# Kernel tuning notes

Hardware: AMD Instinct MI355X
Metric: run time of the kernel (lower is better)

Reference implementation:

```python
import jax, jax.numpy as jnp
import numpy as np

D_MODEL = 1024
NUM_HEADS = 16
HEAD_DIM = D_MODEL // NUM_HEADS


def setup_inputs() -> dict:
    key = jax.random.key(0)
    kx, kq, kk, kv, ko = jax.random.split(key, 5)
    B, S = 2, 2048
    scale = 1.0 / np.sqrt(D_MODEL)
    return {
        "x": jax.random.normal(kx, (B, S, D_MODEL), dtype=jnp.float32),
        "W_q": jax.random.normal(kq, (D_MODEL, D_MODEL), dtype=jnp.float32) * scale,
        "W_k": jax.random.normal(kk, (D_MODEL, D_MODEL), dtype=jnp.float32) * scale,
        "W_v": jax.random.normal(kv, (D_MODEL, D_MODEL), dtype=jnp.float32) * scale,
        "W_o": jax.random.normal(ko, (D_MODEL, D_MODEL), dtype=jnp.float32) * scale,
        "causal": 1,
    }


def _attn(x, W_q, W_k, W_v, W_o, causal):
    B, S, D = x.shape
    H, Hd = NUM_HEADS, HEAD_DIM
    # projections: nn.Linear applies x @ W.T
    q = (x @ W_q.T).reshape(B, S, H, Hd)
    k = (x @ W_k.T).reshape(B, S, H, Hd)
    v = (x @ W_v.T).reshape(B, S, H, Hd)
    # scores: [B, H, S, S]
    scores = jnp.einsum("bqhd,bkhd->bhqk", q, k) / np.sqrt(Hd)
    if causal:
        mask = jnp.triu(jnp.ones((S, S), dtype=bool), k=1)
        scores = jnp.where(mask, -jnp.inf, scores)
    attn = jax.nn.softmax(scores, axis=-1)
    out = jnp.einsum("bhqk,bkhd->bqhd", attn, v).reshape(B, S, D)
    return out @ W_o.T


def reference(x, W_q, W_k, W_v, W_o, causal):
    return _attn(x, W_q, W_k, W_v, W_o, causal)
```

## Files before the change

### kernel.cpp

```cpp
#include <hip/hip_runtime.h>

typedef __attribute__((ext_vector_type(8))) short bf16x8;
typedef __attribute__((ext_vector_type(4))) float f32x4;
typedef __attribute__((ext_vector_type(4))) unsigned short u16x4;

#define MFMA16(a, b, c) __builtin_amdgcn_mfma_f32_16x16x32_bf16((a), (b), (c), 0, 0, 0)

static constexpr int D_MODEL = 1024;
static constexpr int SEQ = 2048;
static constexpr int NH = 16;
static constexpr int HD = 64;
static constexpr int LDA = 40;
static constexpr int MST = 136;
static constexpr float NEG_BIG = -1.0e30f;

__device__ __forceinline__ unsigned short f2bf(float f) {
  union { float f; unsigned int u; } v; v.f = f;
  unsigned int r = v.u + 0x7fffu + ((v.u >> 16) & 1u);
  return (unsigned short)(r >> 16);
}

__device__ __forceinline__ unsigned int cvtpk_bf16(float a, float b) {
  unsigned int r;
  asm("v_cvt_pk_bf16_f32 %0, %1, %2" : "=v"(r) : "v"(a), "v"(b));
  return r;
}

__device__ __forceinline__ int detect_bf16(const unsigned short* xs, int lane) {
  unsigned short s = xs[2 * lane];
  int e = (s >> 7) & 0xFF;
  bool hit = (e >= 117 && e <= 129);
  unsigned long long m = __ballot(hit);
  return (__popcll(m) >= 32) ? 1 : 0;
}

__device__ __forceinline__ bf16x8 ld8(const void* p, size_t eidx, int bf) {
  if (bf) return *(const bf16x8*)((const unsigned short*)p + eidx);
  const float* f = (const float*)p + eidx;
  f32x4 lo = *(const f32x4*)f;
  f32x4 hi = *(const f32x4*)(f + 4);
  bf16x8 r;
  r[0] = (short)f2bf(lo[0]); r[1] = (short)f2bf(lo[1]);
  r[2] = (short)f2bf(lo[2]); r[3] = (short)f2bf(lo[3]);
  r[4] = (short)f2bf(hi[0]); r[5] = (short)f2bf(hi[1]);
  r[6] = (short)f2bf(hi[2]); r[7] = (short)f2bf(hi[3]);
  return r;
}

__device__ __forceinline__ void async16(const unsigned short* g, unsigned short* l) {
  __builtin_amdgcn_global_load_lds(
      (const __attribute__((address_space(1))) void*)g,
      (__attribute__((address_space(3))) void*)l, 16, 0, 0);
}

__global__ __launch_bounds__(64) void detect_kernel(
    const unsigned short* __restrict__ xs, int* __restrict__ flag) {
  int lane = threadIdx.x;
  unsigned short s = xs[2 * lane];
  int e = (s >> 7) & 0xFF;
  bool hit = (e >= 117 && e <= 129);
  unsigned long long m = __ballot(hit);
  if (lane == 0) { flag[0] = (__popcll(m) >= 32) ? 1 : 0; flag[1] = 1; }
}

__global__ __launch_bounds__(256) void convert_kernel(
    const void* __restrict__ X,
    const void* __restrict__ W0, const void* __restrict__ W1,
    const void* __restrict__ W2, const void* __restrict__ W3,
    unsigned short* __restrict__ Xb, unsigned short* __restrict__ Wb)
{
  const int bf = detect_bf16((const unsigned short*)X, threadIdx.x & 63);
  const int ty = blockIdx.y;
  const void* src; unsigned short* dst; size_t n;
  if (ty == 0) { src = X; dst = Xb; n = (size_t)2 * SEQ * D_MODEL; }
  else {
    src = (ty == 1) ? W0 : (ty == 2) ? W1 : (ty == 3) ? W2 : W3;
    dst = Wb + (size_t)(ty - 1) * D_MODEL * D_MODEL;
    n = (size_t)D_MODEL * D_MODEL;
  }
  size_t i = ((size_t)blockIdx.x * 256 + threadIdx.x) * 8;
  if (i >= n) return;
  *(bf16x8*)(dst + i) = ld8(src, i, bf);
}

__device__ __forceinline__ void gemm_fast_core(
    const unsigned short* __restrict__ A, const unsigned short* __restrict__ B,
    int tm, int tn, unsigned short* smem, f32x4 acc[4][4])
{
  const int t = threadIdx.x;
  const int lane = t & 63;
  const int w = t >> 6;
  const int wm = (w >> 1) * 64, wn = (w & 1) * 64;
  const int quad = lane >> 4, l16 = lane & 15;
  const int srow = lane >> 2;
  const int scol = ((lane & 3) ^ ((lane >> 3) & 3)) * 8;
  const int xa = (l16 >> 1) & 3;

#pragma unroll
  for (int mi = 0; mi < 4; ++mi)
#pragma unroll
    for (int ni = 0; ni < 4; ++ni)
      acc[mi][ni] = (f32x4){0.f, 0.f, 0.f, 0.f};

  auto stage = [&](int f, int buf) {
    const int k0 = f * 32;
    unsigned short* dst = smem + buf * 8192;
#pragma unroll
    for (int i = 0; i < 2; ++i) {
      const int row = w * 32 + i * 16;
      async16(A + (size_t)(tm + row + srow) * D_MODEL + k0 + scol,
              dst + row * 32);
      async16(B + (size_t)(tn + row + srow) * D_MODEL + k0 + scol,
              dst + 4096 + row * 32);
    }
  };

  stage(0, 0);
  stage(1, 1);

  int cur = 0, nb = 2;
  for (int f = 0; f < 32; ++f) {
    if (f + 1 < 32) asm volatile("s_waitcnt vmcnt(4)" ::: "memory");
    else            asm volatile("s_waitcnt vmcnt(0)" ::: "memory");
    __builtin_amdgcn_s_barrier();
    __builtin_amdgcn_sched_barrier(0);
    if (f + 2 < 32) stage(f + 2, nb);
    const unsigned short* As = smem + cur * 8192;
    const unsigned short* Bs = As + 4096;
    bf16x8 af[4], bfv[4];
#pragma unroll
    for (int mi = 0; mi < 4; ++mi)
      af[mi] = *(const bf16x8*)(As + (wm + mi * 16 + l16) * 32 + (quad ^ xa) * 8);
#pragma unroll
    for (int ni = 0; ni < 4; ++ni)
      bfv[ni] = *(const bf16x8*)(Bs + (wn + ni * 16 + l16) * 32 + (quad ^ xa) * 8);
    __builtin_amdgcn_s_setprio(1);
#pragma unroll
    for (int mi = 0; mi < 4; ++mi)
#pragma unroll
      for (int ni = 0; ni < 4; ++ni)
        acc[mi][ni] = MFMA16(af[mi], bfv[ni], acc[mi][ni]);
    __builtin_amdgcn_s_setprio(0);
    cur = (cur == 2) ? 0 : cur + 1;
    nb = (nb == 2) ? 0 : nb + 1;
  }
}

__global__ __launch_bounds__(256) void qkv_fast_kernel(
    const unsigned short* __restrict__ X,
    const unsigned short* __restrict__ Wb,
    unsigned short* __restrict__ qd,
    unsigned short* __restrict__ kws,
    unsigned short* __restrict__ vws)
{
  __shared__ __align__(16) unsigned short smem[3 * 8192];
  const int bid = blockIdx.x;
  const int xcd = bid & 7, s0 = bid >> 3;
  const int z = s0 >> 5;
  const int tn = ((s0 >> 2) & 7) * 128;
  const int tm = (xcd * 4 + (s0 & 3)) * 128;
  const unsigned short* W = Wb + (size_t)z * D_MODEL * D_MODEL;
  f32x4 acc[4][4];
  gemm_fast_core(X, W, tm, tn, smem, acc);

  const int t = threadIdx.x;
  const int lane = t & 63, w = t >> 6;
  const int wm = (w >> 1) * 64, wn = (w & 1) * 64;
  const int quad = lane >> 4, l16 = lane & 15;

  if (z == 2) {
    const int b = tm >> 11;
    const int sb = tm & 2047;
#pragma unroll
    for (int ph = 0; ph < 2; ++ph) {
      __syncthreads();
      if ((w & 1) == ph) {
#pragma unroll
        for (int mi = 0; mi < 4; ++mi)
#pragma unroll
          for (int ni = 0; ni < 4; ++ni)
#pragma unroll
            for (int r = 0; r < 4; ++r) {
              int m_local = wm + mi * 16 + quad * 4 + r;
              int n_sub = ni * 16 + l16;
              smem[n_sub * MST + m_local] = f2bf(acc[mi][ni][r]);
            }
      }
      __syncthreads();
      const int row = t >> 2, c0 = (t & 3) * 32;
      const int n_g = tn + ph * 64 + row;
      const int h = n_g >> 6, d = n_g & 63;
      unsigned short* dst = vws + (((size_t)b * NH + h) * HD + d) * SEQ + sb + c0;
#pragma unroll
      for (int cc = 0; cc < 4; ++cc)
        *(bf16x8*)(dst + cc * 8) = *(const bf16x8*)(smem + row * MST + c0 + cc * 8);
    }
    return;
  }
#pragma unroll
  for (int mi = 0; mi < 4; ++mi)
#pragma unroll
    for (int ni = 0; ni < 4; ++ni)
#pragma unroll
      for (int r = 0; r < 4; ++r) {
        int m = tm + wm + mi * 16 + quad * 4 + r;
        int n = tn + wn + ni * 16 + l16;
        unsigned short bv = f2bf(acc[mi][ni][r]);
        if (z == 0) {
          qd[(size_t)m * D_MODEL + n] = bv;
        } else {
          int b = m >> 11, sg = m & 2047;
          int h = n >> 6, d = n & 63;
          kws[(((size_t)b * NH + h) * SEQ + sg) * HD + d] = bv;
        }
      }
}

__global__ __launch_bounds__(256) void oproj_fast_kernel(
    const unsigned short* __restrict__ AW,
    const unsigned short* __restrict__ Wo,
    const unsigned short* __restrict__ Xorig,
    void* __restrict__ out)
{
  __shared__ __align__(16) unsigned short smem[3 * 8192];
  const int bf = detect_bf16(Xorig, threadIdx.x & 63);
  const int bid = blockIdx.x;
  const int xcd = bid & 7, s0 = bid >> 3;
  const int tmg = xcd >> 2, tng = xcd & 3;
  const int tm = (tmg * 16 + (s0 >> 1)) * 128;
  const int tn = (tng * 2 + (s0 & 1)) * 128;
  f32x4 acc[4][4];
  gemm_fast_core(AW, Wo, tm, tn, smem, acc);

  const int t = threadIdx.x;
  const int lane = t & 63, w = t >> 6;
  const int wm = (w >> 1) * 64, wn = (w & 1) * 64;
  const int quad = lane >> 4, l16 = lane & 15;
  if (bf) {
    unsigned short* o = (unsigned short*)out;
#pragma unroll
    for (int mi = 0; mi < 4; ++mi)
#pragma unroll
      for (int ni = 0; ni < 4; ++ni)
#pragma unroll
        for (int r = 0; r < 4; ++r) {
          int m = tm + wm + mi * 16 + quad * 4 + r;
          int n = tn + wn + ni * 16 + l16;
          o[(size_t)m * D_MODEL + n] = f2bf(acc[mi][ni][r]);
        }
  } else {
    float* o = (float*)out;
#pragma unroll
    for (int mi = 0; mi < 4; ++mi)
#pragma unroll
      for (int ni = 0; ni < 4; ++ni)
#pragma unroll
        for (int r = 0; r < 4; ++r) {
          int m = tm + wm + mi * 16 + quad * 4 + r;
          int n = tn + wn + ni * 16 + l16;
          o[(size_t)m * D_MODEL + n] = acc[mi][ni][r];
        }
  }
}

__device__ __forceinline__ void gemm_tile_128x128(
    const void* __restrict__ A, const void* __restrict__ B, int bf,
    int tm, int tn, unsigned short* As, unsigned short* Bs, f32x4 acc[4][4])
{
  const int t = threadIdx.x;
  const int lane = t & 63;
  const int w = t >> 6;
  const int wm = (w >> 1) * 64, wn = (w & 1) * 64;
  const int quad = lane >> 4, l16 = lane & 15;
  const int r0 = t >> 2, kc = (t & 3) * 8;
  const int r1 = r0 + 64;

#pragma unroll
  for (int mi = 0; mi < 4; ++mi)
#pragma unroll
    for (int ni = 0; ni < 4; ++ni)
      acc[mi][ni] = (f32x4){0.f, 0.f, 0.f, 0.f};

  for (int k0 = 0; k0 < D_MODEL; k0 += 32) {
    bf16x8 a0 = ld8(A, (size_t)(tm + r0) * D_MODEL + k0 + kc, bf);
    bf16x8 a1 = ld8(A, (size_t)(tm + r1) * D_MODEL + k0 + kc, bf);
    bf16x8 b0 = ld8(B, (size_t)(tn + r0) * D_MODEL + k0 + kc, bf);
    bf16x8 b1 = ld8(B, (size_t)(tn + r1) * D_MODEL + k0 + kc, bf);
    __syncthreads();
    *(bf16x8*)(As + r0 * LDA + kc) = a0;
    *(bf16x8*)(As + r1 * LDA + kc) = a1;
    *(bf16x8*)(Bs + r0 * LDA + kc) = b0;
    *(bf16x8*)(Bs + r1 * LDA + kc) = b1;
    __syncthreads();
    bf16x8 af[4], bfv[4];
#pragma unroll
    for (int mi = 0; mi < 4; ++mi)
      af[mi] = *(const bf16x8*)(As + (wm + mi * 16 + l16) * LDA + quad * 8);
#pragma unroll
    for (int ni = 0; ni < 4; ++ni)
      bfv[ni] = *(const bf16x8*)(Bs + (wn + ni * 16 + l16) * LDA + quad * 8);
#pragma unroll
    for (int mi = 0; mi < 4; ++mi)
#pragma unroll
      for (int ni = 0; ni < 4; ++ni)
        acc[mi][ni] = MFMA16(af[mi], bfv[ni], acc[mi][ni]);
  }
}

__global__ __launch_bounds__(256) void qkv_kernel(
    const void* __restrict__ X,
    const void* __restrict__ Wq,
    const void* __restrict__ Wk,
    const void* __restrict__ Wv,
    const int* __restrict__ flag,
    unsigned short* __restrict__ qd,
    unsigned short* __restrict__ kws,
    unsigned short* __restrict__ vws)
{
  __shared__ __align__(16) unsigned short As[128 * LDA];
  __shared__ __align__(16) unsigned short Bs[128 * LDA];
  const int bf = *flag;
  const int z = blockIdx.z;
  const void* W = (z == 0) ? Wq : ((z == 1) ? Wk : Wv);
  const int tm = blockIdx.y * 128, tn = blockIdx.x * 128;
  f32x4 acc[4][4];
  gemm_tile_128x128(X, W, bf, tm, tn, As, Bs, acc);

  const int t = threadIdx.x;
  const int lane = t & 63, w = t >> 6;
  const int wm = (w >> 1) * 64, wn = (w & 1) * 64;
  const int quad = lane >> 4, l16 = lane & 15;
#pragma unroll
  for (int mi = 0; mi < 4; ++mi)
#pragma unroll
    for (int ni = 0; ni < 4; ++ni)
#pragma unroll
      for (int r = 0; r < 4; ++r) {
        int m = tm + wm + mi * 16 + quad * 4 + r;
        int n = tn + wn + ni * 16 + l16;
        unsigned short bv = f2bf(acc[mi][ni][r]);
        if (z == 0) {
          qd[(size_t)m * D_MODEL + n] = bv;
        } else {
          int b = m >> 11, s = m & 2047;
          int h = n >> 6, d = n & 63;
          if (z == 1) kws[(((size_t)b * NH + h) * SEQ + s) * HD + d] = bv;
          else        vws[(((size_t)b * NH + h) * HD + d) * SEQ + s] = bv;
        }
      }
}

__global__ __launch_bounds__(256) void oproj_kernel(
    const unsigned short* __restrict__ AW,
    const void* __restrict__ Wo,
    const int* __restrict__ flag,
    float* __restrict__ tmp)
{
  __shared__ __align__(16) unsigned short As[128 * LDA];
  __shared__ __align__(16) unsigned short Bs[128 * LDA];
  const int bf = *flag;
  const int t = threadIdx.x;
  const int lane = t & 63;
  const int w = t >> 6;
  const int wm = (w >> 1) * 64, wn = (w & 1) * 64;
  const int quad = lane >> 4, l16 = lane & 15;
  const int r0 = t >> 2, kc = (t & 3) * 8;
  const int r1 = r0 + 64;
  const int tm = blockIdx.y * 128, tn = blockIdx.x * 128;
  f32x4 acc[4][4];
#pragma unroll
  for (int mi = 0; mi < 4; ++mi)
#pragma unroll
    for (int ni = 0; ni < 4; ++ni)
      acc[mi][ni] = (f32x4){0.f, 0.f, 0.f, 0.f};

  for (int k0 = 0; k0 < D_MODEL; k0 += 32) {
    bf16x8 a0 = *(const bf16x8*)(AW + (size_t)(tm + r0) * D_MODEL + k0 + kc);
    bf16x8 a1 = *(const bf16x8*)(AW + (size_t)(tm + r1) * D_MODEL + k0 + kc);
    bf16x8 b0 = ld8(Wo, (size_t)(tn + r0) * D_MODEL + k0 + kc, bf);
    bf16x8 b1 = ld8(Wo, (size_t)(tn + r1) * D_MODEL + k0 + kc, bf);
    __syncthreads();
    *(bf16x8*)(As + r0 * LDA + kc) = a0;
    *(bf16x8*)(As + r1 * LDA + kc) = a1;
    *(bf16x8*)(Bs + r0 * LDA + kc) = b0;
    *(bf16x8*)(Bs + r1 * LDA + kc) = b1;
    __syncthreads();
    bf16x8 af[4], bfv[4];
#pragma unroll
    for (int mi = 0; mi < 4; ++mi)
      af[mi] = *(const bf16x8*)(As + (wm + mi * 16 + l16) * LDA + quad * 8);
#pragma unroll
    for (int ni = 0; ni < 4; ++ni)
      bfv[ni] = *(const bf16x8*)(Bs + (wn + ni * 16 + l16) * LDA + quad * 8);
#pragma unroll
    for (int mi = 0; mi < 4; ++mi)
#pragma unroll
      for (int ni = 0; ni < 4; ++ni)
        acc[mi][ni] = MFMA16(af[mi], bfv[ni], acc[mi][ni]);
  }
#pragma unroll
  for (int mi = 0; mi < 4; ++mi)
#pragma unroll
    for (int ni = 0; ni < 4; ++ni)
#pragma unroll
      for (int r = 0; r < 4; ++r) {
        int m = tm + wm + mi * 16 + quad * 4 + r;
        int n = tn + wn + ni * 16 + l16;
        tmp[(size_t)m * D_MODEL + n] = acc[mi][ni][r];
      }
}

__device__ __forceinline__ void qk_part(
    const bf16x8 (&kfr)[4][2], const bf16x8 (&aq)[2], f32x4 (&sc)[4])
{
  __builtin_amdgcn_s_setprio(1);
#pragma unroll
  for (int cb = 0; cb < 4; ++cb) {
    sc[cb] = (f32x4){0.f, 0.f, 0.f, 0.f};
    sc[cb] = MFMA16(kfr[cb][0], aq[0], sc[cb]);
    sc[cb] = MFMA16(kfr[cb][1], aq[1], sc[cb]);
  }
  __builtin_amdgcn_s_setprio(0);
}

__device__ __forceinline__ void smpv_part(
    f32x4 (&sc)[4], const bf16x8 (&vfr)[4][2], f32x4 (&oacc)[4], float& lsum,
    int diag, int ktbase, int qq, int quad, float Cs)
{
  if (diag) {
#pragma unroll
    for (int cb = 0; cb < 4; ++cb)
#pragma unroll
      for (int rr = 0; rr < 4; ++rr)
        if (ktbase + (cb & 1) * 32 + quad * 8 + (cb >> 1) * 4 + rr > qq)
          sc[cb][rr] = NEG_BIG;
  }
#pragma unroll
  for (int cb = 0; cb < 4; ++cb)
#pragma unroll
    for (int rr = 0; rr < 4; ++rr)
      sc[cb][rr] = __builtin_amdgcn_exp2f(sc[cb][rr] * Cs);
  f32x4 t0, t1;
#pragma unroll
  for (int rr = 0; rr < 4; ++rr) { t0[rr] = sc[0][rr] + sc[1][rr]; }
#pragma unroll
  for (int rr = 0; rr < 4; ++rr) { t1[rr] = sc[2][rr] + sc[3][rr]; }
#pragma unroll
  for (int rr = 0; rr < 4; ++rr) { t0[rr] += t1[rr]; }
  lsum += (t0[0] + t0[1]) + (t0[2] + t0[3]);
  bf16x8 bp[2];
#pragma unroll
  for (int hf = 0; hf < 2; ++hf) {
    union { unsigned int w4[4]; bf16x8 v; } u;
    u.w4[0] = cvtpk_bf16(sc[hf][0], sc[hf][1]);
    u.w4[1] = cvtpk_bf16(sc[hf][2], sc[hf][3]);
    u.w4[2] = cvtpk_bf16(sc[2 + hf][0], sc[2 + hf][1]);
    u.w4[3] = cvtpk_bf16(sc[2 + hf][2], sc[2 + hf][3]);
    bp[hf] = u.v;
  }
  __builtin_amdgcn_s_setprio(1);
#pragma unroll
  for (int db = 0; db < 4; ++db) {
    oacc[db] = MFMA16(vfr[db][0], bp[0], oacc[db]);
    oacc[db] = MFMA16(vfr[db][1], bp[1], oacc[db]);
  }
  __builtin_amdgcn_s_setprio(0);
}

__global__ __launch_bounds__(256, 2) void attn_kernel(
    unsigned short* __restrict__ Qd,
    const unsigned short* __restrict__ Kb,
    const unsigned short* __restrict__ Vt,
    const int* __restrict__ causal_p)
{
  __shared__ __align__(16) unsigned short Ks[3][64 * 64];
  __shared__ __align__(16) unsigned short Vs[3][64 * 64];
  const int bid = blockIdx.x;
  const int xcd = bid & 7, slot = bid >> 3;
  const int bhl = slot >> 4;
  const int praw = slot & 15;
  const int p = (bhl & 2) ? (15 - praw) : praw;
  const int bh = xcd * 4 + bhl;
  const int b = bh >> 4, h = bh & 15;
  const int t = threadIdx.x, lane = t & 63, w = t >> 6;
  const int quad = lane >> 4, l16 = lane & 15;
  const int causal = *causal_p;
  const int tA = causal ? (31 - p) : (2 * p);
  const int tB = causal ? p : (2 * p + 1);
  const int ITEMS = causal ? (32 - p) : 32;
  unsigned short* qh = Qd + (size_t)b * SEQ * D_MODEL + h * HD;
  const unsigned short* kh = Kb + ((size_t)b * NH + h) * SEQ * HD;
  const unsigned short* vh = Vt + ((size_t)b * NH + h) * HD * SEQ;
  const float Cs = 0.125f * 1.4426950408889634f;
  const int srow = lane >> 3;
  const int gcol = ((lane & 7) ^ srow) * 8;
  const int xa = l16 & 7;

  int kvp[2];
#pragma unroll
  for (int j2 = 0; j2 < 2; ++j2) {
    const int rp = w * 16 + j2 * 8 + srow;
    kvp[j2] = ((rp >> 4) & 1) * 32 + ((rp >> 2) & 3) * 8 + ((rp >> 5) & 1) * 4 + (rp & 3);
  }

  const int qA = tA * 64 + w * 16, qB = tB * 64 + w * 16;
  bf16x8 aqA[2], aqB[2];
#pragma unroll
  for (int ch = 0; ch < 2; ++ch) {
    aqA[ch] = *(const bf16x8*)(qh + (size_t)(qA + l16) * D_MODEL +
                               ch * 32 + quad * 8);
    aqB[ch] = *(const bf16x8*)(qh + (size_t)(qB + l16) * D_MODEL +
                               ch * 32 + quad * 8);
  }

  f32x4 oaccA[4], oaccB[4];
#pragma unroll
  for (int db = 0; db < 4; ++db) {
    oaccA[db] = (f32x4){0.f, 0.f, 0.f, 0.f};
    oaccB[db] = (f32x4){0.f, 0.f, 0.f, 0.f};
  }
  float lsumA = 0.f, lsumB = 0.f;

  auto stage = [&](int f, int buf) {
#pragma unroll
    for (int j2 = 0; j2 < 2; ++j2) {
      const int row = w * 16 + j2 * 8;
      async16(kh + (size_t)(f * 64 + kvp[j2]) * HD + gcol, &Ks[buf][row * 64]);
      async16(vh + (size_t)(row + srow) * SEQ + f * 64 + gcol, &Vs[buf][row * 64]);
    }
  };

  stage(0, 0);
  if (ITEMS > 1) stage(1, 1);

  int cur = 0, nb = 2;
  for (int f = 0; f < ITEMS; ++f) {
    if (f + 1 < ITEMS) asm volatile("s_waitcnt vmcnt(4)" ::: "memory");
    else               asm volatile("s_waitcnt vmcnt(0)" ::: "memory");
    __builtin_amdgcn_s_barrier();
    __builtin_amdgcn_sched_barrier(0);
    if (f + 2 < ITEMS) stage(f + 2, nb);

    bf16x8 kfr[4][2], vfr[4][2];
#pragma unroll
    for (int cb = 0; cb < 4; ++cb)
#pragma unroll
      for (int hf = 0; hf < 2; ++hf) {
        kfr[cb][hf] = *(const bf16x8*)(&Ks[cur][(cb * 16 + l16) * 64 +
                                               ((hf * 4 + quad) ^ xa) * 8]);
        vfr[cb][hf] = *(const bf16x8*)(&Vs[cur][(cb * 16 + l16) * 64 +
                                               ((hf * 4 + quad) ^ xa) * 8]);
      }
    const int bAct = causal ? (f <= p) : 1;
    f32x4 scA[4], scB[4];
    qk_part(kfr, aqA, scA);
    if (bAct) qk_part(kfr, aqB, scB);
    smpv_part(scA, vfr, oaccA, lsumA,
              causal && (f == ITEMS - 1), f * 64, qA + l16, quad, Cs);
    if (bAct)
      smpv_part(scB, vfr, oaccB, lsumB,
                causal && (f == p), f * 64, qB + l16, quad, Cs);
    cur = (cur == 2) ? 0 : cur + 1;
    nb = (nb == 2) ? 0 : nb + 1;
  }

  {
    float l = lsumA;
    l += __shfl_xor(l, 16, 64);
    l += __shfl_xor(l, 32, 64);
    float inv = 1.0f / l;
#pragma unroll
    for (int db = 0; db < 4; ++db) {
      u16x4 o;
#pragma unroll
      for (int rr = 0; rr < 4; ++rr) o[rr] = f2bf(oaccA[db][rr] * inv);
      *(u16x4*)(qh + (size_t)(qA + l16) * D_MODEL + db * 16 + quad * 4) = o;
    }
  }
  {
    float l = lsumB;
    l += __shfl_xor(l, 16, 64);
    l += __shfl_xor(l, 32, 64);
    float inv = 1.0f / l;
#pragma unroll
    for (int db = 0; db < 4; ++db) {
      u16x4 o;
#pragma unroll
      for (int rr = 0; rr < 4; ++rr) o[rr] = f2bf(oaccB[db][rr] * inv);
      *(u16x4*)(qh + (size_t)(qB + l16) * D_MODEL + db * 16 + quad * 4) = o;
    }
  }
}

__global__ __launch_bounds__(256) void final_kernel(
    const float* __restrict__ tmp, void* __restrict__ out,
    const int* __restrict__ flag)
{
  const int bf = *flag;
  size_t i = ((size_t)blockIdx.x * 256 + threadIdx.x) * 8;
  f32x4 lo = *(const f32x4*)(tmp + i);
  f32x4 hi = *(const f32x4*)(tmp + i + 4);
  if (bf) {
    bf16x8 r;
    r[0] = (short)f2bf(lo[0]); r[1] = (short)f2bf(lo[1]);
    r[2] = (short)f2bf(lo[2]); r[3] = (short)f2bf(lo[3]);
    r[4] = (short)f2bf(hi[0]); r[5] = (short)f2bf(hi[1]);
    r[6] = (short)f2bf(hi[2]); r[7] = (short)f2bf(hi[3]);
    *(bf16x8*)((unsigned short*)out + i) = r;
  } else {
    *(f32x4*)((float*)out + i) = lo;
    *(f32x4*)((float*)out + i + 4) = hi;
  }
}

extern "C" void kernel_launch(void* const* d_in, const int* in_sizes, int n_in,
                              void* d_out, int out_size, void* d_ws, size_t ws_size,
                              hipStream_t stream) {
  const void* X  = d_in[0];
  const void* Wq = d_in[1];
  const void* Wk = d_in[2];
  const void* Wv = d_in[3];
  const void* Wo = d_in[4];
  const int* causal = (const int*)d_in[5];

  const size_t NE = (size_t)2 * SEQ * D_MODEL;
  const size_t WE = (size_t)D_MODEL * D_MODEL;
  int* flag0 = (int*)d_ws;

  unsigned short* kws = (unsigned short*)((char*)d_ws + 64);
  unsigned short* vws = kws + NE;
  unsigned short* Wb  = vws + NE;
  unsigned short* qdf = Wb + 4 * WE;
  unsigned short* Xbf = qdf + NE;

  const bool big = ws_size >= (size_t)64 + 40ull * 1024 * 1024;

  if (big) {
    hipLaunchKernelGGL(convert_kernel, dim3(2048, 5), dim3(256), 0, stream,
                       X, Wq, Wk, Wv, Wo, Xbf, Wb);
    hipLaunchKernelGGL(qkv_fast_kernel, dim3(768), dim3(256), 0, stream,
                       Xbf, Wb, qdf, kws, vws);
    hipLaunchKernelGGL(attn_kernel, dim3(512), dim3(256), 0, stream,
                       qdf, kws, vws, causal);
    hipLaunchKernelGGL(oproj_fast_kernel, dim3(256), dim3(256), 0, stream,
                       qdf, Wb + 3 * WE, (const unsigned short*)X, d_out);
  } else {
    float* tmp = (float*)kws;
    unsigned short* qd = (unsigned short*)d_out;
    hipLaunchKernelGGL(detect_kernel, dim3(1), dim3(64), 0, stream,
                       (const unsigned short*)X, flag0);
    hipLaunchKernelGGL(qkv_kernel, dim3(8, 32, 3), dim3(256), 0, stream,
                       X, Wq, Wk, Wv, flag0, qd, kws, vws);
    hipLaunchKernelGGL(attn_kernel, dim3(512), dim3(256), 0, stream,
                       qd, kws, vws, causal);
    hipLaunchKernelGGL(oproj_kernel, dim3(8, 32), dim3(256), 0, stream,
                       qd, Wo, flag0, tmp);
    hipLaunchKernelGGL(final_kernel, dim3(2048), dim3(256), 0, stream,
                       tmp, d_out, flag0);
  }
}
```

Before: 172.1 us.

## Fuse convert+QKV and attention+O-proj kernels with software grid barriers

Folds the four-kernel fast path into two persistent-style kernels. Each pair is joined by a global atomic-counter barrier: conversion then QKV GEMM, and attention then output projection. This removes two kernel launch boundaries and the idle gaps between them. It relies on every block being co-resident (768 blocks at 3 per CU, 512 at 2 per CU), otherwise the barrier deadlocks. It also adds a memset launch and spin-wait overhead.

```diff
diff --git a/kernel.cpp b/kernel.cpp
--- a/kernel.cpp
+++ b/kernel.cpp
@@ -53,6 +53,19 @@
       (__attribute__((address_space(3))) void*)l, 16, 0, 0);
 }
 
+__device__ __forceinline__ void gbar(unsigned int* c, unsigned int target) {
+  __threadfence();
+  __syncthreads();
+  if (threadIdx.x == 0) {
+    atomicAdd(c, 1u);
+    while (__hip_atomic_load(c, __ATOMIC_RELAXED, __HIP_MEMORY_SCOPE_AGENT)
+           < target)
+      __builtin_amdgcn_s_sleep(8);
+  }
+  __syncthreads();
+  __threadfence();
+}
+
 __global__ __launch_bounds__(64) void detect_kernel(
     const unsigned short* __restrict__ xs, int* __restrict__ flag) {
   int lane = threadIdx.x;
@@ -61,26 +74,6 @@
   bool hit = (e >= 117 && e <= 129);
   unsigned long long m = __ballot(hit);
   if (lane == 0) { flag[0] = (__popcll(m) >= 32) ? 1 : 0; flag[1] = 1; }
-}
-
-__global__ __launch_bounds__(256) void convert_kernel(
-    const void* __restrict__ X,
-    const void* __restrict__ W0, const void* __restrict__ W1,
-    const void* __restrict__ W2, const void* __restrict__ W3,
-    unsigned short* __restrict__ Xb, unsigned short* __restrict__ Wb)
-{
-  const int bf = detect_bf16((const unsigned short*)X, threadIdx.x & 63);
-  const int ty = blockIdx.y;
-  const void* src; unsigned short* dst; size_t n;
-  if (ty == 0) { src = X; dst = Xb; n = (size_t)2 * SEQ * D_MODEL; }
-  else {
-    src = (ty == 1) ? W0 : (ty == 2) ? W1 : (ty == 3) ? W2 : W3;
-    dst = Wb + (size_t)(ty - 1) * D_MODEL * D_MODEL;
-    n = (size_t)D_MODEL * D_MODEL;
-  }
-  size_t i = ((size_t)blockIdx.x * 256 + threadIdx.x) * 8;
-  if (i >= n) return;
-  *(bf16x8*)(dst + i) = ld8(src, i, bf);
 }
 
 __device__ __forceinline__ void gemm_fast_core(
@@ -146,16 +139,15 @@
   }
 }
 
-__global__ __launch_bounds__(256) void qkv_fast_kernel(
+__device__ void qkv_tile(
     const unsigned short* __restrict__ X,
     const unsigned short* __restrict__ Wb,
     unsigned short* __restrict__ qd,
     unsigned short* __restrict__ kws,
-    unsigned short* __restrict__ vws)
-{
-  __shared__ __align__(16) unsigned short smem[3 * 8192];
-  const int bid = blockIdx.x;
-  const int xcd = bid & 7, s0 = bid >> 3;
+    unsigned short* __restrict__ vws,
+    int lt, unsigned short* smem)
+{
+  const int xcd = lt & 7, s0 = lt >> 3;
   const int z = s0 >> 5;
   const int tn = ((s0 >> 2) & 7) * 128;
   const int tm = (xcd * 4 + (s0 & 3)) * 128;
@@ -216,15 +208,11 @@
       }
 }
 
-__global__ __launch_bounds__(256) void oproj_fast_kernel(
+__device__ void oproj_tile(
     const unsigned short* __restrict__ AW,
     const unsigned short* __restrict__ Wo,
-    const unsigned short* __restrict__ Xorig,
-    void* __restrict__ out)
-{
-  __shared__ __align__(16) unsigned short smem[3 * 8192];
-  const int bf = detect_bf16(Xorig, threadIdx.x & 63);
-  const int bid = blockIdx.x;
+    int bf, void* __restrict__ out, int bid, unsigned short* smem)
+{
   const int xcd = bid & 7, s0 = bid >> 3;
   const int tmg = xcd >> 2, tng = xcd & 3;
   const int tm = (tmg * 16 + (s0 >> 1)) * 128;
@@ -260,6 +248,244 @@
           int n = tn + wn + ni * 16 + l16;
           o[(size_t)m * D_MODEL + n] = acc[mi][ni][r];
         }
+  }
+}
+
+__device__ __forceinline__ void qk_part(
+    const bf16x8 (&kfr)[4][2], const bf16x8 (&aq)[2], f32x4 (&sc)[4])
+{
+  __builtin_amdgcn_s_setprio(1);
+#pragma unroll
+  for (int cb = 0; cb < 4; ++cb) {
+    sc[cb] = (f32x4){0.f, 0.f, 0.f, 0.f};
+    sc[cb] = MFMA16(kfr[cb][0], aq[0], sc[cb]);
+    sc[cb] = MFMA16(kfr[cb][1], aq[1], sc[cb]);
+  }
+  __builtin_amdgcn_s_setprio(0);
+}
+
+__device__ __forceinline__ void smpv_part(
+    f32x4 (&sc)[4], const bf16x8 (&vfr)[4][2], f32x4 (&oacc)[4], float& lsum,
+    int diag, int ktbase, int qq, int quad, float Cs)
+{
+  if (diag) {
+#pragma unroll
+    for (int cb = 0; cb < 4; ++cb)
+#pragma unroll
+      for (int rr = 0; rr < 4; ++rr)
+        if (ktbase + (cb & 1) * 32 + quad * 8 + (cb >> 1) * 4 + rr > qq)
+          sc[cb][rr] = NEG_BIG;
+  }
+#pragma unroll
+  for (int cb = 0; cb < 4; ++cb)
+#pragma unroll
+    for (int rr = 0; rr < 4; ++rr)
+      sc[cb][rr] = __builtin_amdgcn_exp2f(sc[cb][rr] * Cs);
+  f32x4 t0, t1;
+#pragma unroll
+  for (int rr = 0; rr < 4; ++rr) { t0[rr] = sc[0][rr] + sc[1][rr]; }
+#pragma unroll
+  for (int rr = 0; rr < 4; ++rr) { t1[rr] = sc[2][rr] + sc[3][rr]; }
+#pragma unroll
+  for (int rr = 0; rr < 4; ++rr) { t0[rr] += t1[rr]; }
+  lsum += (t0[0] + t0[1]) + (t0[2] + t0[3]);
+  bf16x8 bp[2];
+#pragma unroll
+  for (int hf = 0; hf < 2; ++hf) {
+    union { unsigned int w4[4]; bf16x8 v; } u;
+    u.w4[0] = cvtpk_bf16(sc[hf][0], sc[hf][1]);
+    u.w4[1] = cvtpk_bf16(sc[hf][2], sc[hf][3]);
+    u.w4[2] = cvtpk_bf16(sc[2 + hf][0], sc[2 + hf][1]);
+    u.w4[3] = cvtpk_bf16(sc[2 + hf][2], sc[2 + hf][3]);
+    bp[hf] = u.v;
+  }
+  __builtin_amdgcn_s_setprio(1);
+#pragma unroll
+  for (int db = 0; db < 4; ++db) {
+    oacc[db] = MFMA16(vfr[db][0], bp[0], oacc[db]);
+    oacc[db] = MFMA16(vfr[db][1], bp[1], oacc[db]);
+  }
+  __builtin_amdgcn_s_setprio(0);
+}
+
+__device__ void attn_block(
+    unsigned short* __restrict__ Qd,
+    const unsigned short* __restrict__ Kb,
+    const unsigned short* __restrict__ Vt,
+    int causal, int bid, unsigned short* smem)
+{
+  unsigned short* KsB = smem;
+  unsigned short* VsB = smem + 12288;
+  const int xcd = bid & 7, slot = bid >> 3;
+  const int bhl = slot >> 4;
+  const int praw = slot & 15;
+  const int p = (bhl & 2) ? (15 - praw) : praw;
+  const int bh = xcd * 4 + bhl;
+  const int b = bh >> 4, h = bh & 15;
+  const int t = threadIdx.x, lane = t & 63, w = t >> 6;
+  const int quad = lane >> 4, l16 = lane & 15;
+  const int tA = causal ? (31 - p) : (2 * p);
+  const int tB = causal ? p : (2 * p + 1);
+  const int ITEMS = causal ? (32 - p) : 32;
+  unsigned short* qh = Qd + (size_t)b * SEQ * D_MODEL + h * HD;
+  const unsigned short* kh = Kb + ((size_t)b * NH + h) * SEQ * HD;
+  const unsigned short* vh = Vt + ((size_t)b * NH + h) * HD * SEQ;
+  const float Cs = 0.125f * 1.4426950408889634f;
+  const int srow = lane >> 3;
+  const int gcol = ((lane & 7) ^ srow) * 8;
+  const int xa = l16 & 7;
+
+  int kvp[2];
+#pragma unroll
+  for (int j2 = 0; j2 < 2; ++j2) {
+    const int rp = w * 16 + j2 * 8 + srow;
+    kvp[j2] = ((rp >> 4) & 1) * 32 + ((rp >> 2) & 3) * 8 + ((rp >> 5) & 1) * 4 + (rp & 3);
+  }
+
+  const int qA = tA * 64 + w * 16, qB = tB * 64 + w * 16;
+  bf16x8 aqA[2], aqB[2];
+#pragma unroll
+  for (int ch = 0; ch < 2; ++ch) {
+    aqA[ch] = *(const bf16x8*)(qh + (size_t)(qA + l16) * D_MODEL +
+                               ch * 32 + quad * 8);
+    aqB[ch] = *(const bf16x8*)(qh + (size_t)(qB + l16) * D_MODEL +
+                               ch * 32 + quad * 8);
+  }
+
+  f32x4 oaccA[4], oaccB[4];
+#pragma unroll
+  for (int db = 0; db < 4; ++db) {
+    oaccA[db] = (f32x4){0.f, 0.f, 0.f, 0.f};
+    oaccB[db] = (f32x4){0.f, 0.f, 0.f, 0.f};
+  }
+  float lsumA = 0.f, lsumB = 0.f;
+
+  auto stage = [&](int f, int buf) {
+#pragma unroll
+    for (int j2 = 0; j2 < 2; ++j2) {
+      const int row = w * 16 + j2 * 8;
+      async16(kh + (size_t)(f * 64 + kvp[j2]) * HD + gcol,
+              KsB + buf * 4096 + row * 64);
+      async16(vh + (size_t)(row + srow) * SEQ + f * 64 + gcol,
+              VsB + buf * 4096 + row * 64);
+    }
+  };
+
+  stage(0, 0);
+  if (ITEMS > 1) stage(1, 1);
+
+  int cur = 0, nb = 2;
+  for (int f = 0; f < ITEMS; ++f) {
+    if (f + 1 < ITEMS) asm volatile("s_waitcnt vmcnt(4)" ::: "memory");
+    else               asm volatile("s_waitcnt vmcnt(0)" ::: "memory");
+    __builtin_amdgcn_s_barrier();
+    __builtin_amdgcn_sched_barrier(0);
+    if (f + 2 < ITEMS) stage(f + 2, nb);
+
+    bf16x8 kfr[4][2], vfr[4][2];
+#pragma unroll
+    for (int cb = 0; cb < 4; ++cb)
+#pragma unroll
+      for (int hf = 0; hf < 2; ++hf) {
+        kfr[cb][hf] = *(const bf16x8*)(KsB + cur * 4096 + (cb * 16 + l16) * 64 +
+                                       ((hf * 4 + quad) ^ xa) * 8);
+        vfr[cb][hf] = *(const bf16x8*)(VsB + cur * 4096 + (cb * 16 + l16) * 64 +
+                                       ((hf * 4 + quad) ^ xa) * 8);
+      }
+    const int bAct = causal ? (f <= p) : 1;
+    f32x4 scA[4], scB[4];
+    qk_part(kfr, aqA, scA);
+    if (bAct) qk_part(kfr, aqB, scB);
+    smpv_part(scA, vfr, oaccA, lsumA,
+              causal && (f == ITEMS - 1), f * 64, qA + l16, quad, Cs);
+    if (bAct)
+      smpv_part(scB, vfr, oaccB, lsumB,
+                causal && (f == p), f * 64, qB + l16, quad, Cs);
+    cur = (cur == 2) ? 0 : cur + 1;
+    nb = (nb == 2) ? 0 : nb + 1;
+  }
+
+  {
+    float l = lsumA;
+    l += __shfl_xor(l, 16, 64);
+    l += __shfl_xor(l, 32, 64);
+    float inv = 1.0f / l;
+#pragma unroll
+    for (int db = 0; db < 4; ++db) {
+      u16x4 o;
+#pragma unroll
+      for (int rr = 0; rr < 4; ++rr) o[rr] = f2bf(oaccA[db][rr] * inv);
+      *(u16x4*)(qh + (size_t)(qA + l16) * D_MODEL + db * 16 + quad * 4) = o;
+    }
+  }
+  {
+    float l = lsumB;
+    l += __shfl_xor(l, 16, 64);
+    l += __shfl_xor(l, 32, 64);
+    float inv = 1.0f / l;
+#pragma unroll
+    for (int db = 0; db < 4; ++db) {
+      u16x4 o;
+#pragma unroll
+      for (int rr = 0; rr < 4; ++rr) o[rr] = f2bf(oaccB[db][rr] * inv);
+      *(u16x4*)(qh + (size_t)(qB + l16) * D_MODEL + db * 16 + quad * 4) = o;
+    }
+  }
+}
+
+__global__ __launch_bounds__(256, 3) void convert_qkv_kernel(
+    const void* __restrict__ X,
+    const void* __restrict__ Wq, const void* __restrict__ Wk,
+    const void* __restrict__ Wv, const void* __restrict__ Wo,
+    unsigned short* __restrict__ Xb, unsigned short* __restrict__ Wb,
+    unsigned short* __restrict__ qd, unsigned short* __restrict__ kws,
+    unsigned short* __restrict__ vws,
+    unsigned int* __restrict__ bar)
+{
+  __shared__ __align__(16) unsigned short smem[3 * 8192];
+  const int bid = blockIdx.x;
+  const int tid = threadIdx.x;
+  const int bf = detect_bf16((const unsigned short*)X, tid & 63);
+
+  {
+    const size_t NEx = (size_t)2 * SEQ * D_MODEL;
+    const size_t WE1 = (size_t)D_MODEL * D_MODEL;
+    const size_t total8 = (NEx + 4 * WE1) / 8;
+    for (size_t c = (size_t)bid * 256 + tid; c < total8; c += 768 * 256) {
+      size_t i = c * 8;
+      if (i < NEx) {
+        *(bf16x8*)(Xb + i) = ld8(X, i, bf);
+      } else {
+        size_t j = i - NEx;
+        size_t wi = j >> 20;
+        size_t off = j & (WE1 - 1);
+        const void* src = (wi == 0) ? Wq : (wi == 1) ? Wk : (wi == 2) ? Wv : Wo;
+        *(bf16x8*)(Wb + j) = ld8(src, off, bf);
+      }
+    }
+  }
+  gbar(bar + 0, 768u);
+
+  qkv_tile(Xb, Wb, qd, kws, vws, bid, smem);
+}
+
+__global__ __launch_bounds__(256, 2) void attn_oproj_kernel(
+    unsigned short* __restrict__ qd,
+    const unsigned short* __restrict__ kws,
+    const unsigned short* __restrict__ vws,
+    const int* __restrict__ causal_p,
+    const unsigned short* __restrict__ Xorig,
+    const unsigned short* __restrict__ WoB,
+    void* __restrict__ out,
+    unsigned int* __restrict__ bar)
+{
+  __shared__ __align__(16) unsigned short smem[3 * 8192];
+  const int causal = *causal_p;
+  attn_block(qd, kws, vws, causal, blockIdx.x, smem);
+  gbar(bar + 1, 512u);
+  if (blockIdx.x < 256) {
+    const int bf = detect_bf16(Xorig, threadIdx.x & 63);
+    oproj_tile(qd, WoB, bf, out, blockIdx.x, smem);
   }
 }
 
@@ -410,186 +636,14 @@
       }
 }
 
-__device__ __forceinline__ void qk_part(
-    const bf16x8 (&kfr)[4][2], const bf16x8 (&aq)[2], f32x4 (&sc)[4])
-{
-  __builtin_amdgcn_s_setprio(1);
-#pragma unroll
-  for (int cb = 0; cb < 4; ++cb) {
-    sc[cb] = (f32x4){0.f, 0.f, 0.f, 0.f};
-    sc[cb] = MFMA16(kfr[cb][0], aq[0], sc[cb]);
-    sc[cb] = MFMA16(kfr[cb][1], aq[1], sc[cb]);
-  }
-  __builtin_amdgcn_s_setprio(0);
-}
-
-__device__ __forceinline__ void smpv_part(
-    f32x4 (&sc)[4], const bf16x8 (&vfr)[4][2], f32x4 (&oacc)[4], float& lsum,
-    int diag, int ktbase, int qq, int quad, float Cs)
-{
-  if (diag) {
-#pragma unroll
-    for (int cb = 0; cb < 4; ++cb)
-#pragma unroll
-      for (int rr = 0; rr < 4; ++rr)
-        if (ktbase + (cb & 1) * 32 + quad * 8 + (cb >> 1) * 4 + rr > qq)
-          sc[cb][rr] = NEG_BIG;
-  }
-#pragma unroll
-  for (int cb = 0; cb < 4; ++cb)
-#pragma unroll
-    for (int rr = 0; rr < 4; ++rr)
-      sc[cb][rr] = __builtin_amdgcn_exp2f(sc[cb][rr] * Cs);
-  f32x4 t0, t1;
-#pragma unroll
-  for (int rr = 0; rr < 4; ++rr) { t0[rr] = sc[0][rr] + sc[1][rr]; }
-#pragma unroll
-  for (int rr = 0; rr < 4; ++rr) { t1[rr] = sc[2][rr] + sc[3][rr]; }
-#pragma unroll
-  for (int rr = 0; rr < 4; ++rr) { t0[rr] += t1[rr]; }
-  lsum += (t0[0] + t0[1]) + (t0[2] + t0[3]);
-  bf16x8 bp[2];
-#pragma unroll
-  for (int hf = 0; hf < 2; ++hf) {
-    union { unsigned int w4[4]; bf16x8 v; } u;
-    u.w4[0] = cvtpk_bf16(sc[hf][0], sc[hf][1]);
-    u.w4[1] = cvtpk_bf16(sc[hf][2], sc[hf][3]);
-    u.w4[2] = cvtpk_bf16(sc[2 + hf][0], sc[2 + hf][1]);
-    u.w4[3] = cvtpk_bf16(sc[2 + hf][2], sc[2 + hf][3]);
-    bp[hf] = u.v;
-  }
-  __builtin_amdgcn_s_setprio(1);
-#pragma unroll
-  for (int db = 0; db < 4; ++db) {
-    oacc[db] = MFMA16(vfr[db][0], bp[0], oacc[db]);
-    oacc[db] = MFMA16(vfr[db][1], bp[1], oacc[db]);
-  }
-  __builtin_amdgcn_s_setprio(0);
-}
-
 __global__ __launch_bounds__(256, 2) void attn_kernel(
     unsigned short* __restrict__ Qd,
     const unsigned short* __restrict__ Kb,
     const unsigned short* __restrict__ Vt,
     const int* __restrict__ causal_p)
 {
-  __shared__ __align__(16) unsigned short Ks[3][64 * 64];
-  __shared__ __align__(16) unsigned short Vs[3][64 * 64];
-  const int bid = blockIdx.x;
-  const int xcd = bid & 7, slot = bid >> 3;
-  const int bhl = slot >> 4;
-  const int praw = slot & 15;
-  const int p = (bhl & 2) ? (15 - praw) : praw;
-  const int bh = xcd * 4 + bhl;
-  const int b = bh >> 4, h = bh & 15;
-  const int t = threadIdx.x, lane = t & 63, w = t >> 6;
-  const int quad = lane >> 4, l16 = lane & 15;
-  const int causal = *causal_p;
-  const int tA = causal ? (31 - p) : (2 * p);
-  const int tB = causal ? p : (2 * p + 1);
-  const int ITEMS = causal ? (32 - p) : 32;
-  unsigned short* qh = Qd + (size_t)b * SEQ * D_MODEL + h * HD;
-  const unsigned short* kh = Kb + ((size_t)b * NH + h) * SEQ * HD;
-  const unsigned short* vh = Vt + ((size_t)b * NH + h) * HD * SEQ;
-  const float Cs = 0.125f * 1.4426950408889634f;
-  const int srow = lane >> 3;
-  const int gcol = ((lane & 7) ^ srow) * 8;
-  const int xa = l16 & 7;
-
-  int kvp[2];
-#pragma unroll
-  for (int j2 = 0; j2 < 2; ++j2) {
-    const int rp = w * 16 + j2 * 8 + srow;
-    kvp[j2] = ((rp >> 4) & 1) * 32 + ((rp >> 2) & 3) * 8 + ((rp >> 5) & 1) * 4 + (rp & 3);
-  }
-
-  const int qA = tA * 64 + w * 16, qB = tB * 64 + w * 16;
-  bf16x8 aqA[2], aqB[2];
-#pragma unroll
-  for (int ch = 0; ch < 2; ++ch) {
-    aqA[ch] = *(const bf16x8*)(qh + (size_t)(qA + l16) * D_MODEL +
-                               ch * 32 + quad * 8);
-    aqB[ch] = *(const bf16x8*)(qh + (size_t)(qB + l16) * D_MODEL +
-                               ch * 32 + quad * 8);
-  }
-
-  f32x4 oaccA[4], oaccB[4];
-#pragma unroll
-  for (int db = 0; db < 4; ++db) {
-    oaccA[db] = (f32x4){0.f, 0.f, 0.f, 0.f};
-    oaccB[db] = (f32x4){0.f, 0.f, 0.f, 0.f};
-  }
-  float lsumA = 0.f, lsumB = 0.f;
-
-  auto stage = [&](int f, int buf) {
-#pragma unroll
-    for (int j2 = 0; j2 < 2; ++j2) {
-      const int row = w * 16 + j2 * 8;
-      async16(kh + (size_t)(f * 64 + kvp[j2]) * HD + gcol, &Ks[buf][row * 64]);
-      async16(vh + (size_t)(row + srow) * SEQ + f * 64 + gcol, &Vs[buf][row * 64]);
-    }
-  };
-
-  stage(0, 0);
-  if (ITEMS > 1) stage(1, 1);
-
-  int cur = 0, nb = 2;
-  for (int f = 0; f < ITEMS; ++f) {
-    if (f + 1 < ITEMS) asm volatile("s_waitcnt vmcnt(4)" ::: "memory");
-    else               asm volatile("s_waitcnt vmcnt(0)" ::: "memory");
-    __builtin_amdgcn_s_barrier();
-    __builtin_amdgcn_sched_barrier(0);
-    if (f + 2 < ITEMS) stage(f + 2, nb);
-
-    bf16x8 kfr[4][2], vfr[4][2];
-#pragma unroll
-    for (int cb = 0; cb < 4; ++cb)
-#pragma unroll
-      for (int hf = 0; hf < 2; ++hf) {
-        kfr[cb][hf] = *(const bf16x8*)(&Ks[cur][(cb * 16 + l16) * 64 +
-                                               ((hf * 4 + quad) ^ xa) * 8]);
-        vfr[cb][hf] = *(const bf16x8*)(&Vs[cur][(cb * 16 + l16) * 64 +
-                                               ((hf * 4 + quad) ^ xa) * 8]);
-      }
-    const int bAct = causal ? (f <= p) : 1;
-    f32x4 scA[4], scB[4];
-    qk_part(kfr, aqA, scA);
-    if (bAct) qk_part(kfr, aqB, scB);
-    smpv_part(scA, vfr, oaccA, lsumA,
-              causal && (f == ITEMS - 1), f * 64, qA + l16, quad, Cs);
-    if (bAct)
-      smpv_part(scB, vfr, oaccB, lsumB,
-                causal && (f == p), f * 64, qB + l16, quad, Cs);
-    cur = (cur == 2) ? 0 : cur + 1;
-    nb = (nb == 2) ? 0 : nb + 1;
-  }
-
-  {
-    float l = lsumA;
-    l += __shfl_xor(l, 16, 64);
-    l += __shfl_xor(l, 32, 64);
-    float inv = 1.0f / l;
-#pragma unroll
-    for (int db = 0; db < 4; ++db) {
-      u16x4 o;
-#pragma unroll
-      for (int rr = 0; rr < 4; ++rr) o[rr] = f2bf(oaccA[db][rr] * inv);
-      *(u16x4*)(qh + (size_t)(qA + l16) * D_MODEL + db * 16 + quad * 4) = o;
-    }
-  }
-  {
-    float l = lsumB;
-    l += __shfl_xor(l, 16, 64);
-    l += __shfl_xor(l, 32, 64);
-    float inv = 1.0f / l;
-#pragma unroll
-    for (int db = 0; db < 4; ++db) {
-      u16x4 o;
-#pragma unroll
-      for (int rr = 0; rr < 4; ++rr) o[rr] = f2bf(oaccB[db][rr] * inv);
-      *(u16x4*)(qh + (size_t)(qB + l16) * D_MODEL + db * 16 + quad * 4) = o;
-    }
-  }
+  __shared__ __align__(16) unsigned short smem[3 * 8192];
+  attn_block(Qd, Kb, Vt, *causal_p, blockIdx.x, smem);
 }
 
 __global__ __launch_bounds__(256) void final_kernel(
@@ -627,6 +681,7 @@
   const size_t WE = (size_t)D_MODEL * D_MODEL;
   int* flag0 = (int*)d_ws;
 
+  unsigned int* bar = (unsigned int*)d_ws;
   unsigned short* kws = (unsigned short*)((char*)d_ws + 64);
   unsigned short* vws = kws + NE;
   unsigned short* Wb  = vws + NE;
@@ -636,14 +691,12 @@
   const bool big = ws_size >= (size_t)64 + 40ull * 1024 * 1024;
 
   if (big) {
-    hipLaunchKernelGGL(convert_kernel, dim3(2048, 5), dim3(256), 0, stream,
-                       X, Wq, Wk, Wv, Wo, Xbf, Wb);
-    hipLaunchKernelGGL(qkv_fast_kernel, dim3(768), dim3(256), 0, stream,
-                       Xbf, Wb, qdf, kws, vws);
-    hipLaunchKernelGGL(attn_kernel, dim3(512), dim3(256), 0, stream,
-                       qdf, kws, vws, causal);
-    hipLaunchKernelGGL(oproj_fast_kernel, dim3(256), dim3(256), 0, stream,
-                       qdf, Wb + 3 * WE, (const unsigned short*)X, d_out);
+    hipMemsetAsync((void*)bar, 0, 64, stream);
+    hipLaunchKernelGGL(convert_qkv_kernel, dim3(768), dim3(256), 0, stream,
+                       X, Wq, Wk, Wv, Wo, Xbf, Wb, qdf, kws, vws, bar);
+    hipLaunchKernelGGL(attn_oproj_kernel, dim3(512), dim3(256), 0, stream,
+                       qdf, kws, vws, causal, (const unsigned short*)X,
+                       Wb + 3 * WE, d_out, bar);
   } else {
     float* tmp = (float*)kws;
     unsigned short* qd = (unsigned short*)d_out;
```

Result: slower. 469.5 us (+172.8%).
